# Kernel tuning notes

Measured on AMD Instinct MI355X. Metric: run time of the kernel, lower is better.

## Reference

```python
import jax, jax.numpy as jnp
import numpy as np

GROUP = 64          # quantization group size along input dim
EPS = 1e-6          # rms_norm_eps
THETA = 1000000.0   # rope theta
NUM_HEADS = 16
NUM_KV_HEADS = 4
HEAD_DIM = 128


def _qlinear(x, wq, s, b=None):
    # dequantize int8-valued weights with per-group scales, then GEMM
    o, i = wq.shape
    w = (wq.reshape(o, i // GROUP, GROUP).astype(jnp.float32) * s[:, :, None]).reshape(o, i)
    y = jnp.einsum('bsi,oi->bso', x, w)
    return y + b if b is not None else y


def _rmsnorm(x, w):
    return x * jax.lax.rsqrt(jnp.mean(x * x, axis=-1, keepdims=True) + EPS) * w


def _rope(x, offset):
    # x: [B, H, S, hd], neox-style half rotation
    hd = x.shape[-1]
    S = x.shape[2]
    pos = (jnp.arange(S) + offset).astype(jnp.float32)
    inv = THETA ** (-(jnp.arange(0, hd, 2).astype(jnp.float32)) / hd)  # [hd/2]
    ang = pos[:, None] * inv[None, :]                                  # [S, hd/2]
    cos, sin = jnp.cos(ang), jnp.sin(ang)
    x1, x2 = x[..., : hd // 2], x[..., hd // 2 :]
    return jnp.concatenate([x1 * cos - x2 * sin, x2 * cos + x1 * sin], axis=-1)


def setup_inputs() -> dict:
    key = jax.random.key(0)
    B, S, D, I = 2, 1024, 2048, 5632
    KV = NUM_KV_HEADS * HEAD_DIM  # 512
    keys = iter(jax.random.split(key, 32))

    def qw(shape):
        return jax.random.randint(next(keys), shape, -127, 128, dtype=jnp.int32)

    def sc(shape):
        return jax.random.uniform(next(keys), shape, jnp.float32, 0.5, 1.5) * 0.001

    inp = {
        'x': jax.random.normal(next(keys), (B, S, D), jnp.float32),
        'wq_q': qw((D, D)),   'wq_s': sc((D, D // GROUP)),
        'bq': jax.random.normal(next(keys), (D,), jnp.float32) * 0.02,
        'wk_q': qw((KV, D)),  'wk_s': sc((KV, D // GROUP)),
        'bk': jax.random.normal(next(keys), (KV,), jnp.float32) * 0.02,
        'wv_q': qw((KV, D)),  'wv_s': sc((KV, D // GROUP)),
        'bv': jax.random.normal(next(keys), (KV,), jnp.float32) * 0.02,
        'wo_q': qw((D, D)),   'wo_s': sc((D, D // GROUP)),
        'gate_q': qw((I, D)), 'gate_s': sc((I, D // GROUP)),
        'up_q': qw((I, D)),   'up_s': sc((I, D // GROUP)),
        'down_q': qw((D, I)), 'down_s': sc((D, I // GROUP)),
        'w_in_ln': jnp.ones((D,), jnp.float32),
        'w_post_ln': jnp.ones((D,), jnp.float32),
        'offset': 0,
    }
    return inp


def reference(x, wq_q, wq_s, bq, wk_q, wk_s, bk, wv_q, wv_s, bv, wo_q, wo_s,
              gate_q, gate_s, up_q, up_s, down_q, down_s, w_in_ln, w_post_ln, offset):
    B, S, D = x.shape
    H, KVH, hd = NUM_HEADS, NUM_KV_HEADS, HEAD_DIM

    # --- attention sub-block ---
    h = _rmsnorm(x, w_in_ln)
    q = _qlinear(h, wq_q, wq_s, bq).reshape(B, S, H, hd).transpose(0, 2, 1, 3)
    k = _qlinear(h, wk_q, wk_s, bk).reshape(B, S, KVH, hd).transpose(0, 2, 1, 3)
    v = _qlinear(h, wv_q, wv_s, bv).reshape(B, S, KVH, hd).transpose(0, 2, 1, 3)
    q = _rope(q, offset)
    k = _rope(k, offset)

    g = H // KVH  # query groups per kv head
    qg = q.reshape(B, KVH, g, S, hd)
    scores = jnp.einsum('bghsd,bgtd->bghst', qg, k) * (1.0 / np.sqrt(hd)).astype(np.float32)
    causal = jnp.tril(jnp.ones((S, S), dtype=bool))  # prefill causal mask (empty cache)
    scores = jnp.where(causal, scores, jnp.float32(-1e9))
    p = jax.nn.softmax(scores, axis=-1)
    o = jnp.einsum('bghst,bgtd->bghsd', p, v)
    o = o.reshape(B, H, S, hd).transpose(0, 2, 1, 3).reshape(B, S, D)
    x = x + _qlinear(o, wo_q, wo_s)

    # --- mlp sub-block ---
    h2 = _rmsnorm(x, w_post_ln)
    gate = jax.nn.silu(_qlinear(h2, gate_q, gate_s))
    up = _qlinear(h2, up_q, up_s)
    mlp = _qlinear(gate * up, down_q, down_s)
    return x + mlp
```

## Files before the change

kernel.cpp:

```cpp
#include <hip/hip_runtime.h>
#include <cstdint>
#include <cstddef>

#define DEV __device__ __forceinline__

typedef _Float16 f16x8 __attribute__((ext_vector_type(8)));
typedef float f32x4 __attribute__((ext_vector_type(4)));

static constexpr int D_MODEL = 2048;
static constexpr int D_FF    = 5632;
static constexpr int N_QKV   = 3072;
static constexpr int SEQ     = 1024;
static constexpr int BATCH   = 2;
static constexpr int ROWS    = BATCH * SEQ;
static constexpr int HEADS   = 16;
static constexpr int HD      = 128;

DEV uint16_t f2h(float f) {
    return __builtin_bit_cast(uint16_t, (_Float16)f);
}

DEV void async_load16(const void* g, void* lds) {
    __builtin_amdgcn_global_load_lds(
        reinterpret_cast<__attribute__((address_space(1))) void*>(
            reinterpret_cast<uintptr_t>(g)),
        reinterpret_cast<__attribute__((address_space(3))) void*>(
            static_cast<uint32_t>(reinterpret_cast<uintptr_t>(lds))),
        16, 0, 0);
}

DEV void dq_body(const int* __restrict__ q, const float* __restrict__ s,
                 uint16_t* __restrict__ out, int I, int mode, int idx)
{
    const int e = idx * 4;
    const int row = e / I;
    const int i = e - row * I;
    const int4 qv = *reinterpret_cast<const int4*>(&q[e]);
    const float scf = s[row * (I >> 6) + (i >> 6)];
    int orow = row;
    if (mode == 1) orow = ((row >> 4) << 5) + (row & 15);
    else if (mode == 2) orow = ((row >> 4) << 5) + (row & 15) + 16;
    uint16_t h[4];
    h[0] = f2h((float)qv.x * scf);
    h[1] = f2h((float)qv.y * scf);
    h[2] = f2h((float)qv.z * scf);
    h[3] = f2h((float)qv.w * scf);
    uint2 pk;
    pk.x = (uint32_t)h[0] | ((uint32_t)h[1] << 16);
    pk.y = (uint32_t)h[2] | ((uint32_t)h[3] << 16);
    *reinterpret_cast<uint2*>(&out[(size_t)orow * I + i]) = pk;
}

__global__ __launch_bounds__(256)
void norm_dqA_kernel(const float* __restrict__ x, const float* __restrict__ wln,
                     uint16_t* __restrict__ outh,
                     const int* __restrict__ wq_q, const float* __restrict__ wq_s,
                     const int* __restrict__ wk_q, const float* __restrict__ wk_s,
                     const int* __restrict__ wv_q, const float* __restrict__ wv_s,
                     const int* __restrict__ wo_q, const float* __restrict__ wo_s,
                     uint16_t* __restrict__ Wqkv, uint16_t* __restrict__ Wo)
{
    __shared__ float red[4];
    const int bid = blockIdx.x;
    const int tid = threadIdx.x;
    if (bid < ROWS) {
        const float* xr = x + (size_t)bid * D_MODEL;
        const float4 v0 = *reinterpret_cast<const float4*>(&xr[tid * 8]);
        const float4 v1 = *reinterpret_cast<const float4*>(&xr[tid * 8 + 4]);
        float ss = v0.x*v0.x + v0.y*v0.y + v0.z*v0.z + v0.w*v0.w
                 + v1.x*v1.x + v1.y*v1.y + v1.z*v1.z + v1.w*v1.w;
#pragma unroll
        for (int off = 32; off; off >>= 1) ss += __shfl_xor(ss, off);
        if ((tid & 63) == 0) red[tid >> 6] = ss;
        __syncthreads();
        const float rms = rsqrtf((red[0] + red[1] + red[2] + red[3]) * (1.0f / D_MODEL) + 1e-6f);
        const int cb = tid * 8;
        const size_t base = (size_t)bid * D_MODEL + cb;
        const float vals[8] = {v0.x, v0.y, v0.z, v0.w, v1.x, v1.y, v1.z, v1.w};
#pragma unroll
        for (int k = 0; k < 8; k += 2) {
            const uint16_t h0 = f2h(vals[k] * rms * wln[cb + k]);
            const uint16_t h1 = f2h(vals[k + 1] * rms * wln[cb + k + 1]);
            *reinterpret_cast<uint32_t*>(&outh[base + k]) = (uint32_t)h0 | ((uint32_t)h1 << 16);
        }
    } else {
        const int b2 = bid - ROWS;
        const int* q; const float* s; uint16_t* out; int seg0;
        if (b2 < 4096)      { q = wq_q; s = wq_s; out = Wqkv;               seg0 = 0; }
        else if (b2 < 5120) { q = wk_q; s = wk_s; out = Wqkv + 2048 * 2048; seg0 = 4096; }
        else if (b2 < 6144) { q = wv_q; s = wv_s; out = Wqkv + 2560 * 2048; seg0 = 5120; }
        else                { q = wo_q; s = wo_s; out = Wo;                 seg0 = 6144; }
        dq_body(q, s, out, 2048, 0, (b2 - seg0) * 256 + tid);
    }
}
static constexpr int NORM_DQA_BLOCKS = ROWS + 10240;

__global__ __launch_bounds__(256)
void rmsnorm_kernel(const float* __restrict__ x, const float* __restrict__ wln,
                    uint16_t* __restrict__ out)
{
    __shared__ float red[4];
    const int row = blockIdx.x;
    const int tid = threadIdx.x;
    const float* xr = x + (size_t)row * D_MODEL;
    const float4 v0 = *reinterpret_cast<const float4*>(&xr[tid * 8]);
    const float4 v1 = *reinterpret_cast<const float4*>(&xr[tid * 8 + 4]);
    float ss = v0.x*v0.x + v0.y*v0.y + v0.z*v0.z + v0.w*v0.w
             + v1.x*v1.x + v1.y*v1.y + v1.z*v1.z + v1.w*v1.w;
#pragma unroll
    for (int off = 32; off; off >>= 1) ss += __shfl_xor(ss, off);
    if ((tid & 63) == 0) red[tid >> 6] = ss;
    __syncthreads();
    const float rms = rsqrtf((red[0] + red[1] + red[2] + red[3]) * (1.0f / D_MODEL) + 1e-6f);
    const int cb = tid * 8;
    const size_t base = (size_t)row * D_MODEL + cb;
    const float vals[8] = {v0.x, v0.y, v0.z, v0.w, v1.x, v1.y, v1.z, v1.w};
#pragma unroll
    for (int k = 0; k < 8; k += 2) {
        const uint16_t h0 = f2h(vals[k] * rms * wln[cb + k]);
        const uint16_t h1 = f2h(vals[k + 1] * rms * wln[cb + k + 1]);
        *reinterpret_cast<uint32_t*>(&out[base + k]) = (uint32_t)h0 | ((uint32_t)h1 << 16);
    }
}

__global__ __launch_bounds__(256)
void gemm_f16_glu_kernel(const uint16_t* __restrict__ A, const uint16_t* __restrict__ W,
                         uint16_t* __restrict__ outh, int M, int N, int K)
{
    __shared__ uint16_t sA[2][128 * 64];
    __shared__ uint16_t sB[2][128 * 64];

    const int tid  = threadIdx.x;
    const int lane = tid & 63;
    const int wv   = tid >> 6;
    const int wm   = wv >> 1;
    const int wn   = wv & 1;
    const int quad = lane >> 4;
    const int l16  = lane & 15;

    const int nBn = N >> 7;
    const int bm  = blockIdx.x / nBn;
    const int bn  = blockIdx.x - bm * nBn;
    const int m0  = bm << 7;
    const int n0  = bn << 7;

    f32x4 acc[4][4];
#pragma unroll
    for (int i = 0; i < 4; i++)
#pragma unroll
        for (int j = 0; j < 4; j++)
            acc[i][j] = (f32x4){0.f, 0.f, 0.f, 0.f};

    const uint16_t* Ab = A + (size_t)m0 * K;
    const uint16_t* Wb = W + (size_t)n0 * K;

    auto stage = [&](int kt, int bsel) {
#pragma unroll
        for (int p = 0; p < 4; p++) {
            const int cb = p * 256 + wv * 64;
            const int c  = cb + lane;
            const int row = c >> 3;
            const int g   = (c & 7) ^ (row & 7);
            const size_t goff = (size_t)row * K + kt + g * 8;
            async_load16(Ab + goff, &sA[bsel][cb * 8]);
            async_load16(Wb + goff, &sB[bsel][cb * 8]);
        }
    };

    stage(0, 0);
    __syncthreads();

    const int nKt = K >> 6;
    for (int t = 0; t < nKt; t++) {
        const int cur = t & 1;
        if (t + 1 < nKt) stage((t + 1) << 6, cur ^ 1);
        const uint16_t* sAc = sA[cur];
        const uint16_t* sBc = sB[cur];
#pragma unroll
        for (int kk = 0; kk < 2; kk++) {
            const int gsw = ((kk * 4 + quad) ^ (l16 & 7)) * 8;
            f16x8 bfv[4];
#pragma unroll
            for (int j = 0; j < 4; j++)
                bfv[j] = *reinterpret_cast<const f16x8*>(
                    &sBc[(wn * 64 + j * 16 + l16) * 64 + gsw]);
#pragma unroll
            for (int i = 0; i < 4; i++) {
                const f16x8 af = *reinterpret_cast<const f16x8*>(
                    &sAc[(wm * 64 + i * 16 + l16) * 64 + gsw]);
#pragma unroll
                for (int j = 0; j < 4; j++)
                    acc[i][j] = __builtin_amdgcn_mfma_f32_16x16x32_f16(af, bfv[j], acc[i][j], 0, 0, 0);
            }
        }
        __syncthreads();
    }

    const int NH = N >> 1;
#pragma unroll
    for (int i = 0; i < 4; i++) {
        const int rowb = m0 + wm * 64 + i * 16 + quad * 4;
#pragma unroll
        for (int r = 0; r < 4; r++) {
            const size_t rr = (size_t)(rowb + r);
#pragma unroll
            for (int pjt = 0; pjt < 2; pjt++) {
                const float g = acc[i][2 * pjt][r];
                const float u = acc[i][2 * pjt + 1][r];
                const float a = (g / (1.0f + __expf(-g))) * u;
                const int cc = (n0 >> 1) + wn * 32 + pjt * 16 + l16;
                outh[rr * NH + cc] = f2h(a);
            }
        }
    }
}

__global__ __launch_bounds__(256)
void gemm_f16_m64_kernel(const uint16_t* __restrict__ A, const uint16_t* __restrict__ W,
                         const float* __restrict__ bq, const float* __restrict__ bk,
                         const float* __restrict__ bv, const float* __restrict__ resid,
                         float* __restrict__ outf, int M, int N, int K)
{
    __shared__ uint16_t sA[2][64 * 64];
    __shared__ uint16_t sB[2][128 * 64];

    const int tid  = threadIdx.x;
    const int lane = tid & 63;
    const int wv   = tid >> 6;
    const int quad = lane >> 4;
    const int l16  = lane & 15;

    const int nBn = N >> 7;
    const int bm  = blockIdx.x / nBn;
    const int bn  = blockIdx.x - bm * nBn;
    const int m0  = bm << 6;
    const int n0  = bn << 7;

    f32x4 acc[4][2];
#pragma unroll
    for (int i = 0; i < 4; i++)
#pragma unroll
        for (int j = 0; j < 2; j++)
            acc[i][j] = (f32x4){0.f, 0.f, 0.f, 0.f};

    const uint16_t* Ab = A + (size_t)m0 * K;
    const uint16_t* Wb = W + (size_t)n0 * K;

    auto stage = [&](int kt, int bsel) {
#pragma unroll
        for (int p = 0; p < 2; p++) {
            const int cb = p * 256 + wv * 64;
            const int c  = cb + lane;
            const int row = c >> 3;
            const int g   = (c & 7) ^ (row & 7);
            async_load16(Ab + (size_t)row * K + kt + g * 8, &sA[bsel][cb * 8]);
        }
#pragma unroll
        for (int p = 0; p < 4; p++) {
            const int cb = p * 256 + wv * 64;
            const int c  = cb + lane;
            const int row = c >> 3;
            const int g   = (c & 7) ^ (row & 7);
            async_load16(Wb + (size_t)row * K + kt + g * 8, &sB[bsel][cb * 8]);
        }
    };

    stage(0, 0);
    __syncthreads();

    const int nKt = K >> 6;
    for (int t = 0; t < nKt; t++) {
        const int cur = t & 1;
        if (t + 1 < nKt) stage((t + 1) << 6, cur ^ 1);
        const uint16_t* sAc = sA[cur];
        const uint16_t* sBc = sB[cur];
#pragma unroll
        for (int kk = 0; kk < 2; kk++) {
            const int gsw = ((kk * 4 + quad) ^ (l16 & 7)) * 8;
            f16x8 bfv[2];
#pragma unroll
            for (int j = 0; j < 2; j++)
                bfv[j] = *reinterpret_cast<const f16x8*>(
                    &sBc[(wv * 32 + j * 16 + l16) * 64 + gsw]);
#pragma unroll
            for (int i = 0; i < 4; i++) {
                const f16x8 af = *reinterpret_cast<const f16x8*>(
                    &sAc[(i * 16 + l16) * 64 + gsw]);
#pragma unroll
                for (int j = 0; j < 2; j++)
                    acc[i][j] = __builtin_amdgcn_mfma_f32_16x16x32_f16(af, bfv[j], acc[i][j], 0, 0, 0);
            }
        }
        __syncthreads();
    }

#pragma unroll
    for (int i = 0; i < 4; i++) {
        const int rowb = m0 + i * 16 + quad * 4;
#pragma unroll
        for (int r = 0; r < 4; r++) {
            const size_t rr = (size_t)(rowb + r);
#pragma unroll
            for (int j = 0; j < 2; j++) {
                const int cc = n0 + wv * 32 + j * 16 + l16;
                float v = acc[i][j][r];
                if (bq) {
                    float bb;
                    if (cc < 2048)      bb = bq[cc];
                    else if (cc < 2560) bb = bk[cc - 2048];
                    else                bb = bv[cc - 2560];
                    v += bb;
                }
                if (resid) v += resid[rr * N + cc];
                outf[rr * N + cc] = v;
            }
        }
    }
}

static constexpr int ROPE_Q_THREADS = ROWS * 16 * 64;
static constexpr int ROPE_THREADS   = ROPE_Q_THREADS + ROWS * 4 * 64;
static constexpr int PREPV_BLOCKS   = BATCH * 4 * (SEQ / 64);
static constexpr int ROPE_PREP_BLOCKS = PREPV_BLOCKS + ROPE_THREADS / 256;
static constexpr float LOG2_1E6_OVER_64 = 0.31143075889910283f;

__global__ __launch_bounds__(256)
void rope_prep_kernel(const float* __restrict__ qkv, const int* __restrict__ offp,
                      uint16_t* __restrict__ Qb, uint16_t* __restrict__ Kb,
                      uint16_t* __restrict__ Vt)
{
    __shared__ uint16_t sh[128 * 72];
    const int tid = threadIdx.x;
    if (blockIdx.x < PREPV_BLOCKS) {
        const int sc  = blockIdx.x & 15;
        const int bk  = blockIdx.x >> 4;
        const int b   = bk >> 2, kvh = bk & 3;
#pragma unroll
        for (int p = 0; p < 8; p++) {
            const int q4 = p * 256 + tid;
            const int sloc = q4 >> 5, d4 = (q4 & 31) * 4;
            const float4 v = *reinterpret_cast<const float4*>(
                &qkv[(size_t)(b * SEQ + sc * 64 + sloc) * N_QKV + 2560 + kvh * HD + d4]);
            sh[(d4 + 0) * 72 + sloc] = f2h(v.x);
            sh[(d4 + 1) * 72 + sloc] = f2h(v.y);
            sh[(d4 + 2) * 72 + sloc] = f2h(v.z);
            sh[(d4 + 3) * 72 + sloc] = f2h(v.w);
        }
        __syncthreads();
        const int d = tid >> 1, half = tid & 1;
        const size_t ob = ((size_t)(bk * 128 + d)) * SEQ + sc * 64 + half * 32;
        const uint16_t* srh = &sh[d * 72 + half * 32];
#pragma unroll
        for (int k = 0; k < 4; k++)
            *reinterpret_cast<uint4*>(&Vt[ob + k * 8]) =
                *reinterpret_cast<const uint4*>(&srh[k * 8]);
        return;
    }
    const int gidx = (blockIdx.x - PREPV_BLOCKS) * 256 + tid;
    if (gidx < ROPE_Q_THREADS) {
        const int idx = gidx;
        const int d   = idx & 63;
        const int h   = (idx >> 6) & 15;
        const int row = idx >> 10;
        const int b   = row >> 10;
        const int s   = row & (SEQ - 1);
        const float pos  = (float)(s + *offp);
        const float freq = exp2f(-(float)d * LOG2_1E6_OVER_64);
        float sn, cs;
        __sincosf(pos * freq, &sn, &cs);
        const size_t gb = (size_t)row * N_QKV + h * HD + d;
        const float x1 = qkv[gb];
        const float x2 = qkv[gb + 64];
        const float qscale = 0.08838834764831845f;
        const size_t ob = ((size_t)(b * 16 + h) * SEQ + s) * HD + d;
        Qb[ob]      = f2h((x1 * cs - x2 * sn) * qscale);
        Qb[ob + 64] = f2h((x2 * cs + x1 * sn) * qscale);
    } else {
        const int idx = gidx - ROPE_Q_THREADS;
        const int d   = idx & 63;
        const int kvh = (idx >> 6) & 3;
        const int row = idx >> 8;
        const int b   = row >> 10;
        const int s   = row & (SEQ - 1);
        const float pos  = (float)(s + *offp);
        const float freq = exp2f(-(float)d * LOG2_1E6_OVER_64);
        float sn, cs;
        __sincosf(pos * freq, &sn, &cs);
        const size_t gb = (size_t)row * N_QKV + 2048 + kvh * HD + d;
        const float x1 = qkv[gb];
        const float x2 = qkv[gb + 64];
        const size_t ob = ((size_t)(b * 4 + kvh) * SEQ + s) * HD + d;
        Kb[ob]      = f2h(x1 * cs - x2 * sn);
        Kb[ob + 64] = f2h(x2 * cs + x1 * sn);
    }
}

static constexpr int ATTN_BLOCKS   = BATCH * HEADS * (SEQ / 64);
static constexpr int DQB_BLOCKS    = 3 * 11264;
static constexpr int ATTN_DQ_BLOCKS = ATTN_BLOCKS + DQB_BLOCKS;

__global__ __launch_bounds__(256)
void attn_dqB_kernel(const uint16_t* __restrict__ Qb, const uint16_t* __restrict__ Kb,
                     const uint16_t* __restrict__ Vt, uint16_t* __restrict__ att,
                     const int* __restrict__ gate_q, const float* __restrict__ gate_s,
                     const int* __restrict__ up_q, const float* __restrict__ up_s,
                     const int* __restrict__ down_q, const float* __restrict__ down_s,
                     uint16_t* __restrict__ Wgu, uint16_t* __restrict__ Wdown)
{
    __shared__ uint16_t sK[2][32 * 128];
    __shared__ uint16_t sV[2][128 * 32];
    __shared__ uint16_t sP[4 * 16 * 32];

    const int tid  = threadIdx.x;

    if (blockIdx.x >= ATTN_BLOCKS) {
        const int b2 = blockIdx.x - ATTN_BLOCKS;
        if (b2 < 11264)       dq_body(gate_q, gate_s, Wgu,   2048, 1, b2 * 256 + tid);
        else if (b2 < 22528)  dq_body(up_q,   up_s,   Wgu,   2048, 2, (b2 - 11264) * 256 + tid);
        else                  dq_body(down_q, down_s, Wdown, 5632, 0, (b2 - 22528) * 256 + tid);
        return;
    }

    const int lane = tid & 63;
    const int wv   = tid >> 6;
    const int quad = lane >> 4;
    const int l16  = lane & 15;
    const int qsw  = (quad ^ ((l16 >> 1) & 3)) * 8;

    const int bi  = blockIdx.x;
    const int sc  = 15 - (bi >> 5);
    const int bh  = bi & 31;
    const int b   = bh >> 4;
    const int h   = bh & 15;
    const int kvh = h >> 2;
    const int s0  = sc << 6;

    f16x8 qf[4];
    {
        const size_t qb = ((size_t)(b * 16 + h) * SEQ + s0 + wv * 16 + l16) * HD;
#pragma unroll
        for (int ks = 0; ks < 4; ks++)
            qf[ks] = *reinterpret_cast<const f16x8*>(&Qb[qb + ks * 32 + quad * 8]);
    }

    float m_i[4], l_i[4];
#pragma unroll
    for (int r = 0; r < 4; r++) { m_i[r] = -1e30f; l_i[r] = 0.f; }
    f32x4 oacc[8];
#pragma unroll
    for (int dt = 0; dt < 8; dt++) oacc[dt] = (f32x4){0.f, 0.f, 0.f, 0.f};

    const size_t kb = (size_t)(b * 4 + kvh) * SEQ * HD;
    const size_t vb = (size_t)(b * 4 + kvh) * HD * SEQ;

    auto stageKV = [&](int t0, int bsel) {
#pragma unroll
        for (int p = 0; p < 2; p++) {
            const int cb = p * 256 + wv * 64;
            const int c  = cb + lane;
            const int krow = c >> 4;
            const int kcc  = (c & 15) ^ (krow & 7);
            async_load16(Kb + kb + (size_t)(t0 + krow) * HD + kcc * 8, &sK[bsel][cb * 8]);
            const int vrow = c >> 2;
            const int vcc  = (c & 3) ^ ((vrow >> 1) & 3);
            async_load16(Vt + vb + (size_t)vrow * SEQ + t0 + vcc * 8, &sV[bsel][cb * 8]);
        }
    };

    const int ntiles = 2 * sc + 2;
    stageKV(0, 0);
    __syncthreads();

    for (int tt = 0; tt < ntiles; tt++) {
        const int t0 = tt << 5;
        const int cur = tt & 1;
        if (tt + 1 < ntiles) stageKV((tt + 1) << 5, cur ^ 1);

        f32x4 sacc[2];
        sacc[0] = (f32x4){0.f, 0.f, 0.f, 0.f};
        sacc[1] = (f32x4){0.f, 0.f, 0.f, 0.f};
#pragma unroll
        for (int ks = 0; ks < 4; ks++) {
#pragma unroll
            for (int jt = 0; jt < 2; jt++) {
                const int idx = (jt * 16 + l16) * 128 + (((ks * 4 + quad) ^ (l16 & 7)) * 8);
                const f16x8 kf = *reinterpret_cast<const f16x8*>(&sK[cur][idx]);
                sacc[jt] = __builtin_amdgcn_mfma_f32_16x16x32_f16(qf[ks], kf, sacc[jt], 0, 0, 0);
            }
        }

        if (t0 >= s0) {
            const int rowg = s0 + wv * 16 + quad * 4;
#pragma unroll
            for (int jt = 0; jt < 2; jt++) {
                const int key = t0 + jt * 16 + l16;
#pragma unroll
                for (int r = 0; r < 4; r++)
                    if (key > rowg + r) sacc[jt][r] = -1e30f;
            }
        }

        float alpha[4];
#pragma unroll
        for (int r = 0; r < 4; r++) {
            float mt = fmaxf(sacc[0][r], sacc[1][r]);
#pragma unroll
            for (int off = 8; off; off >>= 1) mt = fmaxf(mt, __shfl_xor(mt, off));
            const float mn = fmaxf(m_i[r], mt);
            alpha[r] = __expf(m_i[r] - mn);
            const float p0 = __expf(sacc[0][r] - mn);
            const float p1 = __expf(sacc[1][r] - mn);
            float ps = p0 + p1;
#pragma unroll
            for (int off = 8; off; off >>= 1) ps += __shfl_xor(ps, off);
            l_i[r] = l_i[r] * alpha[r] + ps;
            m_i[r] = mn;
            const int prow = quad * 4 + r;
            sP[wv * 512 + prow * 32 + 0 * 16 + l16] = f2h(p0);
            sP[wv * 512 + prow * 32 + 1 * 16 + l16] = f2h(p1);
        }

#pragma unroll
        for (int dt = 0; dt < 8; dt++) {
#pragma unroll
            for (int r = 0; r < 4; r++) oacc[dt][r] *= alpha[r];
        }
        const f16x8 pf = *reinterpret_cast<const f16x8*>(&sP[wv * 512 + l16 * 32 + quad * 8]);
#pragma unroll
        for (int dt = 0; dt < 8; dt++) {
            const f16x8 vf = *reinterpret_cast<const f16x8*>(&sV[cur][(dt * 16 + l16) * 32 + qsw]);
            oacc[dt] = __builtin_amdgcn_mfma_f32_16x16x32_f16(pf, vf, oacc[dt], 0, 0, 0);
        }

        __syncthreads();
    }

    float inv[4];
#pragma unroll
    for (int r = 0; r < 4; r++) inv[r] = 1.0f / l_i[r];
#pragma unroll
    for (int r = 0; r < 4; r++) {
        const size_t rowg = (size_t)(b * SEQ + s0 + wv * 16 + quad * 4 + r);
#pragma unroll
        for (int dt = 0; dt < 8; dt++)
            att[rowg * D_MODEL + h * HD + dt * 16 + l16] = f2h(oacc[dt][r] * inv[r]);
    }
}

extern "C" void kernel_launch(void* const* d_in, const int* in_sizes, int n_in,
                              void* d_out, int out_size, void* d_ws, size_t ws_size,
                              hipStream_t stream)
{
    (void)in_sizes; (void)n_in; (void)out_size; (void)ws_size;
    const float* x      = (const float*)d_in[0];
    const int*   wq_q   = (const int*)d_in[1];
    const float* wq_s   = (const float*)d_in[2];
    const float* bq     = (const float*)d_in[3];
    const int*   wk_q   = (const int*)d_in[4];
    const float* wk_s   = (const float*)d_in[5];
    const float* bk     = (const float*)d_in[6];
    const int*   wv_q   = (const int*)d_in[7];
    const float* wv_s   = (const float*)d_in[8];
    const float* bv     = (const float*)d_in[9];
    const int*   wo_q   = (const int*)d_in[10];
    const float* wo_s   = (const float*)d_in[11];
    const int*   gate_q = (const int*)d_in[12];
    const float* gate_s = (const float*)d_in[13];
    const int*   up_q   = (const int*)d_in[14];
    const float* up_s   = (const float*)d_in[15];
    const int*   down_q = (const int*)d_in[16];
    const float* down_s = (const float*)d_in[17];
    const float* w_in   = (const float*)d_in[18];
    const float* w_post = (const float*)d_in[19];
    const int*   offp   = (const int*)d_in[20];

    char* p = (char*)d_ws;
    auto alloc = [&](size_t bytes) {
        char* r = p;
        p += (bytes + 255) & ~(size_t)255;
        return r;
    };
    uint16_t* Wgu   = (uint16_t*)alloc((size_t)2 * D_FF * D_MODEL * 2);
    uint16_t* Wdown = (uint16_t*)alloc((size_t)D_MODEL * D_FF * 2);
    uint16_t* hbuf  = (uint16_t*)alloc((size_t)ROWS * D_MODEL * 2);
    float*    x2    = (float*)alloc((size_t)ROWS * D_MODEL * 4);
    char* zone = alloc((size_t)N_QKV * D_MODEL * 2 +
                       (size_t)D_MODEL * D_MODEL * 2 +
                       (size_t)ROWS * N_QKV * 4 + 8192);
    uint16_t* Wqkv = (uint16_t*)zone;
    uint16_t* Wo   = Wqkv + (size_t)N_QKV * D_MODEL;
    float*    qkv  = (float*)(Wo + (size_t)D_MODEL * D_MODEL);
    uint16_t* Qb = Wqkv;
    uint16_t* Kb = Qb + (size_t)BATCH * 16 * SEQ * HD;
    uint16_t* Vt = Kb + (size_t)BATCH * 4 * SEQ * HD;
    uint16_t* att = (uint16_t*)qkv;
    uint16_t* act = (uint16_t*)zone;

    norm_dqA_kernel<<<NORM_DQA_BLOCKS, 256, 0, stream>>>(
        x, w_in, hbuf, wq_q, wq_s, wk_q, wk_s, wv_q, wv_s, wo_q, wo_s, Wqkv, Wo);

    gemm_f16_m64_kernel<<<(ROWS / 64) * (N_QKV / 128), 256, 0, stream>>>(
        hbuf, Wqkv, bq, bk, bv, nullptr, qkv, ROWS, N_QKV, D_MODEL);

    rope_prep_kernel<<<ROPE_PREP_BLOCKS, 256, 0, stream>>>(qkv, offp, Qb, Kb, Vt);

    attn_dqB_kernel<<<ATTN_DQ_BLOCKS, 256, 0, stream>>>(
        Qb, Kb, Vt, att, gate_q, gate_s, up_q, up_s, down_q, down_s, Wgu, Wdown);

    gemm_f16_m64_kernel<<<(ROWS / 64) * (D_MODEL / 128), 256, 0, stream>>>(
        att, Wo, nullptr, nullptr, nullptr, x, x2, ROWS, D_MODEL, D_MODEL);

    rmsnorm_kernel<<<ROWS, 256, 0, stream>>>(x2, w_post, hbuf);

    gemm_f16_glu_kernel<<<(ROWS / 128) * (2 * D_FF / 128), 256, 0, stream>>>(
        hbuf, Wgu, act, ROWS, 2 * D_FF, D_MODEL);

    gemm_f16_m64_kernel<<<(ROWS / 64) * (D_MODEL / 128), 256, 0, stream>>>(
        act, Wdown, nullptr, nullptr, nullptr, x2, (float*)d_out, ROWS, D_MODEL, D_FF);
}
```

Baseline: 519.0 us.

## Switch GEMM kernels to 3-stage K=32 pipeline with explicit vmcnt waits

After: 576.3 us. 11.0% more time.

```diff
diff --git a/kernel.cpp b/kernel.cpp
--- a/kernel.cpp
+++ b/kernel.cpp
@@ -123,12 +123,29 @@
     }
 }
 
+#define PIPE_WAIT_BARRIER(Lcnt)                                         \
+    do {                                                                \
+        if ((Lcnt) == 0) asm volatile("s_waitcnt vmcnt(0)" ::: "memory"); \
+        else if ((Lcnt) == 3) asm volatile("s_waitcnt vmcnt(3)" ::: "memory"); \
+        else asm volatile("s_waitcnt vmcnt(4)" ::: "memory");           \
+        __builtin_amdgcn_s_barrier();                                   \
+        asm volatile("" ::: "memory");                                  \
+        __builtin_amdgcn_sched_barrier(0);                              \
+    } while (0)
+
+#define PIPE_END_BARRIER()                                              \
+    do {                                                                \
+        __builtin_amdgcn_sched_barrier(0);                              \
+        asm volatile("" ::: "memory");                                  \
+        __builtin_amdgcn_s_barrier();                                   \
+    } while (0)
+
 __global__ __launch_bounds__(256)
 void gemm_f16_glu_kernel(const uint16_t* __restrict__ A, const uint16_t* __restrict__ W,
                          uint16_t* __restrict__ outh, int M, int N, int K)
 {
-    __shared__ uint16_t sA[2][128 * 64];
-    __shared__ uint16_t sB[2][128 * 64];
+    __shared__ uint16_t sA[3][128 * 32];
+    __shared__ uint16_t sB[3][128 * 32];
 
     const int tid  = threadIdx.x;
     const int lane = tid & 63;
@@ -154,46 +171,47 @@
     const uint16_t* Ab = A + (size_t)m0 * K;
     const uint16_t* Wb = W + (size_t)n0 * K;
 
-    auto stage = [&](int kt, int bsel) {
-#pragma unroll
-        for (int p = 0; p < 4; p++) {
+    auto stage = [&](int kt, int s) {
+#pragma unroll
+        for (int p = 0; p < 2; p++) {
             const int cb = p * 256 + wv * 64;
             const int c  = cb + lane;
-            const int row = c >> 3;
-            const int g   = (c & 7) ^ (row & 7);
+            const int row = c >> 2;
+            const int g   = (c & 3) ^ ((row >> 1) & 3);
             const size_t goff = (size_t)row * K + kt + g * 8;
-            async_load16(Ab + goff, &sA[bsel][cb * 8]);
-            async_load16(Wb + goff, &sB[bsel][cb * 8]);
+            async_load16(Ab + goff, &sA[s][cb * 8]);
+            async_load16(Wb + goff, &sB[s][cb * 8]);
         }
     };
 
+    const int nKt = K >> 5;
     stage(0, 0);
-    __syncthreads();
-
-    const int nKt = K >> 6;
+    stage(32, 1);
+
+    const int gsw = (quad ^ ((l16 >> 1) & 3)) * 8;
+
     for (int t = 0; t < nKt; t++) {
-        const int cur = t & 1;
-        if (t + 1 < nKt) stage((t + 1) << 6, cur ^ 1);
-        const uint16_t* sAc = sA[cur];
-        const uint16_t* sBc = sB[cur];
-#pragma unroll
-        for (int kk = 0; kk < 2; kk++) {
-            const int gsw = ((kk * 4 + quad) ^ (l16 & 7)) * 8;
-            f16x8 bfv[4];
+        const int s = t % 3;
+        PIPE_WAIT_BARRIER(t + 1 < nKt ? 4 : 0);
+
+        const uint16_t* sAc = sA[s];
+        const uint16_t* sBc = sB[s];
+        f16x8 bfv[4];
+#pragma unroll
+        for (int j = 0; j < 4; j++)
+            bfv[j] = *reinterpret_cast<const f16x8*>(
+                &sBc[(wn * 64 + j * 16 + l16) * 32 + gsw]);
+#pragma unroll
+        for (int i = 0; i < 4; i++) {
+            const f16x8 af = *reinterpret_cast<const f16x8*>(
+                &sAc[(wm * 64 + i * 16 + l16) * 32 + gsw]);
 #pragma unroll
             for (int j = 0; j < 4; j++)
-                bfv[j] = *reinterpret_cast<const f16x8*>(
-                    &sBc[(wn * 64 + j * 16 + l16) * 64 + gsw]);
-#pragma unroll
-            for (int i = 0; i < 4; i++) {
-                const f16x8 af = *reinterpret_cast<const f16x8*>(
-                    &sAc[(wm * 64 + i * 16 + l16) * 64 + gsw]);
-#pragma unroll
-                for (int j = 0; j < 4; j++)
-                    acc[i][j] = __builtin_amdgcn_mfma_f32_16x16x32_f16(af, bfv[j], acc[i][j], 0, 0, 0);
-            }
-        }
-        __syncthreads();
+                acc[i][j] = __builtin_amdgcn_mfma_f32_16x16x32_f16(af, bfv[j], acc[i][j], 0, 0, 0);
+        }
+
+        PIPE_END_BARRIER();
+        if (t + 2 < nKt) stage((t + 2) << 5, (t + 2) % 3);
     }
 
     const int NH = N >> 1;
@@ -221,8 +239,8 @@
                          const float* __restrict__ bv, const float* __restrict__ resid,
                          float* __restrict__ outf, int M, int N, int K)
 {
-    __shared__ uint16_t sA[2][64 * 64];
-    __shared__ uint16_t sB[2][128 * 64];
+    __shared__ uint16_t sA[3][64 * 32];
+    __shared__ uint16_t sB[3][128 * 32];
 
     const int tid  = threadIdx.x;
     const int lane = tid & 63;
@@ -246,52 +264,52 @@
     const uint16_t* Ab = A + (size_t)m0 * K;
     const uint16_t* Wb = W + (size_t)n0 * K;
 
-    auto stage = [&](int kt, int bsel) {
+    auto stage = [&](int kt, int s) {
+        {
+            const int cb = wv * 64;
+            const int c  = cb + lane;
+            const int row = c >> 2;
+            const int g   = (c & 3) ^ ((row >> 1) & 3);
+            async_load16(Ab + (size_t)row * K + kt + g * 8, &sA[s][cb * 8]);
+        }
 #pragma unroll
         for (int p = 0; p < 2; p++) {
             const int cb = p * 256 + wv * 64;
             const int c  = cb + lane;
-            const int row = c >> 3;
-            const int g   = (c & 7) ^ (row & 7);
-            async_load16(Ab + (size_t)row * K + kt + g * 8, &sA[bsel][cb * 8]);
-        }
-#pragma unroll
-        for (int p = 0; p < 4; p++) {
-            const int cb = p * 256 + wv * 64;
-            const int c  = cb + lane;
-            const int row = c >> 3;
-            const int g   = (c & 7) ^ (row & 7);
-            async_load16(Wb + (size_t)row * K + kt + g * 8, &sB[bsel][cb * 8]);
+            const int row = c >> 2;
+            const int g   = (c & 3) ^ ((row >> 1) & 3);
+            async_load16(Wb + (size_t)row * K + kt + g * 8, &sB[s][cb * 8]);
         }
     };
 
+    const int nKt = K >> 5;
     stage(0, 0);
-    __syncthreads();
-
-    const int nKt = K >> 6;
+    stage(32, 1);
+
+    const int gsw = (quad ^ ((l16 >> 1) & 3)) * 8;
+
     for (int t = 0; t < nKt; t++) {
-        const int cur = t & 1;
-        if (t + 1 < nKt) stage((t + 1) << 6, cur ^ 1);
-        const uint16_t* sAc = sA[cur];
-        const uint16_t* sBc = sB[cur];
-#pragma unroll
-        for (int kk = 0; kk < 2; kk++) {
-            const int gsw = ((kk * 4 + quad) ^ (l16 & 7)) * 8;
-            f16x8 bfv[2];
+        const int s = t % 3;
+        PIPE_WAIT_BARRIER(t + 1 < nKt ? 3 : 0);
+
+        const uint16_t* sAc = sA[s];
+        const uint16_t* sBc = sB[s];
+        f16x8 bfv[2];
+#pragma unroll
+        for (int j = 0; j < 2; j++)
+            bfv[j] = *reinterpret_cast<const f16x8*>(
+                &sBc[(wv * 32 + j * 16 + l16) * 32 + gsw]);
+#pragma unroll
+        for (int i = 0; i < 4; i++) {
+            const f16x8 af = *reinterpret_cast<const f16x8*>(
+                &sAc[(i * 16 + l16) * 32 + gsw]);
 #pragma unroll
             for (int j = 0; j < 2; j++)
-                bfv[j] = *reinterpret_cast<const f16x8*>(
-                    &sBc[(wv * 32 + j * 16 + l16) * 64 + gsw]);
-#pragma unroll
-            for (int i = 0; i < 4; i++) {
-                const f16x8 af = *reinterpret_cast<const f16x8*>(
-                    &sAc[(i * 16 + l16) * 64 + gsw]);
-#pragma unroll
-                for (int j = 0; j < 2; j++)
-                    acc[i][j] = __builtin_amdgcn_mfma_f32_16x16x32_f16(af, bfv[j], acc[i][j], 0, 0, 0);
-            }
-        }
-        __syncthreads();
+                acc[i][j] = __builtin_amdgcn_mfma_f32_16x16x32_f16(af, bfv[j], acc[i][j], 0, 0, 0);
+        }
+
+        PIPE_END_BARRIER();
+        if (t + 2 < nKt) stage((t + 2) << 5, (t + 2) % 3);
     }
 
 #pragma unroll
```
